# Kernel optimization log

Hardware: AMD Instinct MI355X
Metric: run time of the kernel (lower is better)

Reference implementation:

```python
import jax, jax.numpy as jnp
import numpy as np

D_MODEL = 768
NUM_HEADS = 12
D_K = D_MODEL // NUM_HEADS  # 64


def setup_inputs() -> dict:
    key = jax.random.key(0)
    ks = jax.random.split(key, 7)
    B, S = 2, 4096
    Q = jax.random.normal(ks[0], (B, S, D_MODEL), dtype=jnp.float32)
    K = jax.random.normal(ks[1], (B, S, D_MODEL), dtype=jnp.float32)
    V = jax.random.normal(ks[2], (B, S, D_MODEL), dtype=jnp.float32)
    scale = 1.0 / np.sqrt(D_MODEL)
    # Per-head projection weights stacked: [H, d_model, d_k] (equivalent to
    # the torch per-head nn.Linear(d_model, d_k, bias=False) applied as x @ W)
    WQ = jax.random.normal(ks[3], (NUM_HEADS, D_MODEL, D_K), dtype=jnp.float32) * scale
    WK = jax.random.normal(ks[4], (NUM_HEADS, D_MODEL, D_K), dtype=jnp.float32) * scale
    WV = jax.random.normal(ks[5], (NUM_HEADS, D_MODEL, D_K), dtype=jnp.float32) * scale
    # Output projection: [num_head*d_v, d_model]
    WO = jax.random.normal(ks[6], (NUM_HEADS * D_K, D_MODEL), dtype=jnp.float32) * scale
    return {"Q": Q, "K": K, "V": V, "WQ": WQ, "WK": WK, "WV": WV, "WO": WO}


def reference(Q, K, V, WQ, WK, WV, WO):
    # Per-head projections (batched over heads): [B,H,S,d_k]
    q = jnp.einsum('bsd,hdk->bhsk', Q, WQ)
    k = jnp.einsum('bsd,hdk->bhsk', K, WK)
    v = jnp.einsum('bsd,hdk->bhsk', V, WV)
    # Full attention scores: [B,H,S,S]
    scores = jnp.einsum('bhqd,bhsd->bhqs', q, k) / jnp.sqrt(jnp.asarray(D_K, q.dtype))
    attn = jax.nn.softmax(scores, axis=-1)  # dropout_p=0 -> identity
    out = jnp.einsum('bhqs,bhsd->bhqd', attn, v)  # [B,H,S,d_k]
    # Concatenate heads along feature dim (head order = concat order)
    B, H, S, Dk = out.shape
    out = out.transpose(0, 2, 1, 3).reshape(B, S, H * Dk)
    return out @ WO  # [B,S,d_model]
```

## Files before the change

kernel.cpp:

```cpp
#include <hip/hip_runtime.h>
#include <hip/hip_bf16.h>
#include <stdint.h>
#include <stddef.h>

#define NH 12
#define DKH 64
#define DM 768
#define SS 4096

typedef __attribute__((ext_vector_type(8))) short bf16x8;
typedef __attribute__((ext_vector_type(4))) float f32x4;
typedef __attribute__((ext_vector_type(16))) float f32x16;

__device__ __forceinline__ unsigned short f2bf(float x) {
  union { float f; unsigned int u; } a; a.f = x;
  unsigned int r = a.u + 0x7fffu + ((a.u >> 16) & 1u);
  return (unsigned short)(r >> 16);
}

__device__ __forceinline__ unsigned pkbf2(float a, float b) {
  union { __hip_bfloat162 h; unsigned u; } x;
  x.h = __float22bfloat162_rn(float2{a, b});
  return x.u;
}

__device__ __forceinline__ unsigned cvt_pk_bf16(float lo, float hi) {
  unsigned r;
  asm("v_cvt_pk_bf16_f32 %0, %1, %2" : "=v"(r) : "v"(lo), "v"(hi));
  return r;
}

__device__ __forceinline__ void plane32_swap(unsigned& a, unsigned& b) {
  asm("v_permlane32_swap_b32 %0, %1" : "+v"(a), "+v"(b));
}

__device__ __forceinline__ float fast_exp2(float x) {
#if __has_builtin(__builtin_amdgcn_exp2f)
  return __builtin_amdgcn_exp2f(x);
#else
  return exp2f(x);
#endif
}

__device__ __forceinline__ void gload16(const void* g, void* l) {
  __builtin_amdgcn_global_load_lds(
      (const __attribute__((address_space(1))) void*)g,
      (__attribute__((address_space(3))) void*)l, 16, 0, 0);
}

__global__ __launch_bounds__(256) void conv_weights(
    const float* __restrict__ WQ, const float* __restrict__ WK,
    const float* __restrict__ WV, const float* __restrict__ WO,
    unsigned short* __restrict__ wq, unsigned short* __restrict__ wk,
    unsigned short* __restrict__ wv, unsigned short* __restrict__ wo) {
  int idx = blockIdx.x * 256 + threadIdx.x;
  if (idx >= DM * DM) return;
  int n = idx / DM, k = idx % DM;
  int src = ((n >> 6) * DM + k) * DKH + (n & 63);
  wq[idx] = f2bf(WQ[src] * 0.18033688011112042f);
  wk[idx] = f2bf(WK[src]);
  wv[idx] = f2bf(WV[src]);
  wo[idx] = f2bf(WO[k * DM + n]);
}

__global__ __launch_bounds__(256) void qkv_conv(
    const float* __restrict__ Q, const float* __restrict__ K,
    const float* __restrict__ V, unsigned short* __restrict__ out) {
  int gid = blockIdx.x * 256 + threadIdx.x;
  int t = gid / 786432, e = gid % 786432;
  const float* src = (t == 0) ? Q : (t == 1) ? K : V;
  float4 a = *(const float4*)(src + (size_t)e * 8);
  float4 c = *(const float4*)(src + (size_t)e * 8 + 4);
  union { unsigned u[4]; uint4 v; } o;
  o.u[0] = pkbf2(a.x, a.y); o.u[1] = pkbf2(a.z, a.w);
  o.u[2] = pkbf2(c.x, c.y); o.u[3] = pkbf2(c.z, c.w);
  *(uint4*)(out + (size_t)t * 6291456 + (size_t)e * 8) = o.v;
}

__global__ __launch_bounds__(256, 2) void proj_gemm3(
    const unsigned short* __restrict__ Abase,
    const unsigned short* __restrict__ Wbase,
    unsigned short* __restrict__ Obase) {
  __shared__ unsigned short As[2][128 * 64];
  __shared__ unsigned short Bs[2][96 * 64];
  const int tid = threadIdx.x;
  const int lane = tid & 63, wave = tid >> 6;
  const int wm = wave >> 1, wn = wave & 1;
  const int l15 = lane & 15, lhi = lane >> 4;
  const int lrow = lane >> 3;
  const int schunk = (lane & 7) ^ lrow;

  int fid = blockIdx.x + (blockIdx.y << 3) + (blockIdx.z << 9);
  int nid = (fid & 7) * 192 + (fid >> 3);
  const int bx = nid & 7;
  const int rem = nid >> 3;
  const int by = rem & 63, z = rem >> 6;
  const bool z2 = (z == 2);

  const unsigned short* A = Abase + (size_t)z * 6291456;
  const unsigned short* Wt = Wbase + (size_t)z * DM * DM;
  unsigned short* out = Obase + (size_t)z * 2 * NH * SS * DKH;
  const int m0 = by * 128, n0 = bx * 96;

  auto stage = [&](int k0, int buf) {
#pragma unroll
    for (int i = 0; i < 4; ++i) {
      int r = wave * 32 + i * 8;
      gload16(A + (size_t)(m0 + r + lrow) * DM + k0 + schunk * 8, &As[buf][r * 64]);
    }
#pragma unroll
    for (int i = 0; i < 3; ++i) {
      int r = wave * 24 + i * 8;
      gload16(Wt + (size_t)(n0 + r + lrow) * DM + k0 + schunk * 8, &Bs[buf][r * 64]);
    }
  };

  f32x4 acc[4][3] = {};

  stage(0, 0);
  stage(64, 1);

  for (int t = 0; t < 12; ++t) {
    if (t < 11) asm volatile("s_waitcnt vmcnt(7)" ::: "memory");
    else        asm volatile("s_waitcnt vmcnt(0)" ::: "memory");
    asm volatile("s_barrier" ::: "memory");
    const int buf = t & 1;
    bf16x8 af[4][2], bfr[3][2];
#pragma unroll
    for (int m = 0; m < 4; ++m) {
      int row = wm * 64 + m * 16 + l15;
#pragma unroll
      for (int ks = 0; ks < 2; ++ks)
        af[m][ks] = *(const bf16x8*)&As[buf][row * 64 + (((ks * 4 + lhi) ^ (row & 7)) * 8)];
    }
#pragma unroll
    for (int n = 0; n < 3; ++n) {
      int row = wn * 48 + n * 16 + l15;
#pragma unroll
      for (int ks = 0; ks < 2; ++ks)
        bfr[n][ks] = *(const bf16x8*)&Bs[buf][row * 64 + (((ks * 4 + lhi) ^ (row & 7)) * 8)];
    }
    asm volatile("s_waitcnt lgkmcnt(0)" ::: "memory");
    asm volatile("s_barrier" ::: "memory");
    if (t + 2 < 12) stage((t + 2) * 64, buf);
    __builtin_amdgcn_s_setprio(1);
#pragma unroll
    for (int ks = 0; ks < 2; ++ks)
#pragma unroll
      for (int m = 0; m < 4; ++m)
#pragma unroll
        for (int n = 0; n < 3; ++n) {
          if (z2)
            acc[m][n] = __builtin_amdgcn_mfma_f32_16x16x32_bf16(bfr[n][ks], af[m][ks], acc[m][n], 0, 0, 0);
          else
            acc[m][n] = __builtin_amdgcn_mfma_f32_16x16x32_bf16(af[m][ks], bfr[n][ks], acc[m][n], 0, 0, 0);
        }
    __builtin_amdgcn_s_setprio(0);
  }

  if (!z2) {
#pragma unroll
    for (int m = 0; m < 4; ++m) {
#pragma unroll
      for (int r = 0; r < 4; ++r) {
        int row = m0 + wm * 64 + m * 16 + lhi * 4 + r;
        int bb = row >> 12, s = row & 4095;
#pragma unroll
        for (int n = 0; n < 3; ++n) {
          int col = n0 + wn * 48 + n * 16 + l15;
          int hh = col >> 6, dk = col & 63;
          out[((size_t)(bb * NH + hh) * SS + s) * DKH + dk] = f2bf(acc[m][n][r]);
        }
      }
    }
  } else {
#pragma unroll
    for (int m = 0; m < 4; ++m) {
      int srow = m0 + wm * 64 + m * 16 + l15;
      int bb = srow >> 12, s = srow & 4095;
#pragma unroll
      for (int n = 0; n < 3; ++n) {
#pragma unroll
        for (int r = 0; r < 4; ++r) {
          int col = n0 + wn * 48 + n * 16 + lhi * 4 + r;
          int hh = col >> 6, dk = col & 63;
          out[((size_t)(bb * NH + hh) * DKH + dk) * SS + s] = f2bf(acc[m][n][r]);
        }
      }
    }
  }
}

__device__ __forceinline__ void pack_pb(const f32x16& s0, const f32x16& s1, bf16x8* pb) {
#pragma unroll
  for (int h2 = 0; h2 < 2; ++h2) {
    unsigned c0a = cvt_pk_bf16(s0[8 * h2 + 0], s0[8 * h2 + 1]);
    unsigned c1a = cvt_pk_bf16(s0[8 * h2 + 2], s0[8 * h2 + 3]);
    unsigned c0b = cvt_pk_bf16(s0[8 * h2 + 4], s0[8 * h2 + 5]);
    unsigned c1b = cvt_pk_bf16(s0[8 * h2 + 6], s0[8 * h2 + 7]);
    plane32_swap(c0a, c0b);
    plane32_swap(c1a, c1b);
    union { unsigned u[4]; bf16x8 v; } f;
    f.u[0] = c0a; f.u[1] = c1a; f.u[2] = c0b; f.u[3] = c1b;
    pb[h2] = f.v;
  }
#pragma unroll
  for (int h2 = 0; h2 < 2; ++h2) {
    unsigned c0a = cvt_pk_bf16(s1[8 * h2 + 0], s1[8 * h2 + 1]);
    unsigned c1a = cvt_pk_bf16(s1[8 * h2 + 2], s1[8 * h2 + 3]);
    unsigned c0b = cvt_pk_bf16(s1[8 * h2 + 4], s1[8 * h2 + 5]);
    unsigned c1b = cvt_pk_bf16(s1[8 * h2 + 6], s1[8 * h2 + 7]);
    plane32_swap(c0a, c0b);
    plane32_swap(c1a, c1b);
    union { unsigned u[4]; bf16x8 v; } f;
    f.u[0] = c0a; f.u[1] = c1a; f.u[2] = c0b; f.u[3] = c1b;
    pb[2 + h2] = f.v;
  }
}

__device__ __forceinline__ float tree16(const f32x16& v) {
  float a = (v[0] + v[1]) + (v[2] + v[3]);
  float b = (v[4] + v[5]) + (v[6] + v[7]);
  float c = (v[8] + v[9]) + (v[10] + v[11]);
  float d = (v[12] + v[13]) + (v[14] + v[15]);
  return (a + b) + (c + d);
}

__global__ __launch_bounds__(128, 2) void flash_attn(
    const unsigned short* __restrict__ Qp, const unsigned short* __restrict__ Kp,
    const unsigned short* __restrict__ Vt, unsigned short* __restrict__ Ao) {
  __shared__ unsigned short KV[2][8192];
  const int tid = threadIdx.x;
  const int lane = tid & 63, wp = tid >> 6;
  const int ql = lane & 31, hi = lane >> 5;

  int fid = blockIdx.x + (blockIdx.y << 5);
  int nid = (fid & 7) * 96 + (fid >> 3);
  const int bx = nid & 31, bh = nid >> 5;
  const int b = bh / NH, h = bh % NH;
  const int q0 = bx * 128 + wp * 64;

  bf16x8 qf0[4], qf1[4];
  {
    const unsigned short* qb = Qp + ((size_t)bh * SS + q0 + ql) * DKH;
#pragma unroll
    for (int s = 0; s < 4; ++s) {
      qf0[s] = *(const bf16x8*)(qb + s * 16 + hi * 8);
      qf1[s] = *(const bf16x8*)(qb + 32 * DKH + s * 16 + hi * 8);
    }
  }

  const unsigned short* gK = Kp + (size_t)bh * SS * DKH;
  const unsigned short* gV = Vt + (size_t)bh * DKH * SS;
  const int lrow = lane >> 3;
  const int sch = ((lane & 7) ^ lrow) * 8;
  const int xs = (ql & 7) << 3;

  auto stage = [&](int kv0, int buf) {
#pragma unroll
    for (int i = 0; i < 4; ++i) {
      int r = wp * 32 + i * 8;
      gload16(gK + (size_t)(kv0 + r + lrow) * DKH + sch, &KV[buf][r * 64]);
      gload16(gV + (size_t)(r + lrow) * SS + kv0 + sch, &KV[buf][4096 + r * 64]);
    }
  };

  stage(0, 0);

  f32x16 oA = {}, oB = {}, oC = {}, oD = {};
  float lp0 = 0.f, lp1 = 0.f;

  for (int it = 0; it < 64; ++it) {
    asm volatile("s_waitcnt vmcnt(0)" ::: "memory");
    __builtin_amdgcn_s_barrier();
    __builtin_amdgcn_sched_barrier(0);
    const int buf = it & 1;
    if (it + 1 < 64) stage((it + 1) * 64, buf ^ 1);
    const unsigned short* Ks = &KV[buf][0];
    const unsigned short* Vs = &KV[buf][4096];

    f32x16 s00 = {}, s01 = {}, s10 = {}, s11 = {};
    __builtin_amdgcn_s_setprio(1);
#pragma unroll
    for (int s = 0; s < 4; ++s) {
      bf16x8 ka0 = *(const bf16x8*)&Ks[ql * 64 + ((s * 16 + hi * 8) ^ xs)];
      bf16x8 ka1 = *(const bf16x8*)&Ks[(32 + ql) * 64 + ((s * 16 + hi * 8) ^ xs)];
      s00 = __builtin_amdgcn_mfma_f32_32x32x16_bf16(ka0, qf0[s], s00, 0, 0, 0);
      s10 = __builtin_amdgcn_mfma_f32_32x32x16_bf16(ka0, qf1[s], s10, 0, 0, 0);
      s01 = __builtin_amdgcn_mfma_f32_32x32x16_bf16(ka1, qf0[s], s01, 0, 0, 0);
      s11 = __builtin_amdgcn_mfma_f32_32x32x16_bf16(ka1, qf1[s], s11, 0, 0, 0);
    }
    __builtin_amdgcn_s_setprio(0);

#pragma unroll
    for (int r = 0; r < 16; ++r) s00[r] = fast_exp2(s00[r]);
#pragma unroll
    for (int r = 0; r < 16; ++r) s01[r] = fast_exp2(s01[r]);
#pragma unroll
    for (int r = 0; r < 16; ++r) s10[r] = fast_exp2(s10[r]);
#pragma unroll
    for (int r = 0; r < 16; ++r) s11[r] = fast_exp2(s11[r]);
    lp0 += tree16(s00) + tree16(s01);
    lp1 += tree16(s10) + tree16(s11);

    bf16x8 pb0[4], pb1[4];
    pack_pb(s00, s01, pb0);
    pack_pb(s10, s11, pb1);

    __builtin_amdgcn_s_setprio(1);
#pragma unroll
    for (int ks = 0; ks < 4; ++ks) {
      bf16x8 va0 = *(const bf16x8*)&Vs[ql * 64 + ((ks * 16 + hi * 8) ^ xs)];
      bf16x8 va1 = *(const bf16x8*)&Vs[(32 + ql) * 64 + ((ks * 16 + hi * 8) ^ xs)];
      oA = __builtin_amdgcn_mfma_f32_32x32x16_bf16(va0, pb0[ks], oA, 0, 0, 0);
      oB = __builtin_amdgcn_mfma_f32_32x32x16_bf16(va1, pb0[ks], oB, 0, 0, 0);
      oC = __builtin_amdgcn_mfma_f32_32x32x16_bf16(va0, pb1[ks], oC, 0, 0, 0);
      oD = __builtin_amdgcn_mfma_f32_32x32x16_bf16(va1, pb1[ks], oD, 0, 0, 0);
    }
    __builtin_amdgcn_s_setprio(0);
  }

  float inv0 = 1.0f / (lp0 + __shfl_xor(lp0, 32));
  float inv1 = 1.0f / (lp1 + __shfl_xor(lp1, 32));
  unsigned short* orow0 = Ao + ((size_t)b * SS + q0 + ql) * DM + h * DKH;
  unsigned short* orow1 = Ao + ((size_t)b * SS + q0 + 32 + ql) * DM + h * DKH;
#pragma unroll
  for (int g = 0; g < 4; ++g) {
    int d0 = g * 8 + hi * 4;
    *(unsigned*)&orow0[d0]          = cvt_pk_bf16(oA[4 * g + 0] * inv0, oA[4 * g + 1] * inv0);
    *(unsigned*)&orow0[d0 + 2]      = cvt_pk_bf16(oA[4 * g + 2] * inv0, oA[4 * g + 3] * inv0);
    *(unsigned*)&orow0[32 + d0]     = cvt_pk_bf16(oB[4 * g + 0] * inv0, oB[4 * g + 1] * inv0);
    *(unsigned*)&orow0[32 + d0 + 2] = cvt_pk_bf16(oB[4 * g + 2] * inv0, oB[4 * g + 3] * inv0);
    *(unsigned*)&orow1[d0]          = cvt_pk_bf16(oC[4 * g + 0] * inv1, oC[4 * g + 1] * inv1);
    *(unsigned*)&orow1[d0 + 2]      = cvt_pk_bf16(oC[4 * g + 2] * inv1, oC[4 * g + 3] * inv1);
    *(unsigned*)&orow1[32 + d0]     = cvt_pk_bf16(oD[4 * g + 0] * inv1, oD[4 * g + 1] * inv1);
    *(unsigned*)&orow1[32 + d0 + 2] = cvt_pk_bf16(oD[4 * g + 2] * inv1, oD[4 * g + 3] * inv1);
  }
}

__global__ __launch_bounds__(256, 2) void out_gemm(
    const unsigned short* __restrict__ A, const unsigned short* __restrict__ Wt,
    float* __restrict__ out) {
  __shared__ unsigned short As[2][64 * 64];
  __shared__ unsigned short Bs[2][128 * 64];
  const int tid = threadIdx.x;
  const int lane = tid & 63, wave = tid >> 6;
  const int wm = wave >> 1, wn = wave & 1;
  const int l15 = lane & 15, lhi = lane >> 4;
  const int lrow = lane >> 3;
  const int schunk = (lane & 7) ^ lrow;

  int fid = blockIdx.x + 6 * blockIdx.y;
  int nid = (fid & 7) * 96 + (fid >> 3);
  const int bx = nid % 6, by = nid / 6;
  const int m0 = by * 64, n0 = bx * 128;

  auto stage = [&](int k0, int buf) {
#pragma unroll
    for (int i = 0; i < 4; ++i) {
      int r = wave * 32 + i * 8;
      gload16(Wt + (size_t)(n0 + r + lrow) * DM + k0 + schunk * 8, &Bs[buf][r * 64]);
    }
#pragma unroll
    for (int i = 0; i < 2; ++i) {
      int r = wave * 16 + i * 8;
      gload16(A + (size_t)(m0 + r + lrow) * DM + k0 + schunk * 8, &As[buf][r * 64]);
    }
  };

  f32x4 acc[2][4] = {};
  stage(0, 0);
  stage(64, 1);

  for (int t = 0; t < 12; ++t) {
    if (t < 11) asm volatile("s_waitcnt vmcnt(6)" ::: "memory");
    else        asm volatile("s_waitcnt vmcnt(0)" ::: "memory");
    asm volatile("s_barrier" ::: "memory");
    const int buf = t & 1;
    bf16x8 af[2][2], bfr[4][2];
#pragma unroll
    for (int m = 0; m < 2; ++m) {
      int row = wm * 32 + m * 16 + l15;
#pragma unroll
      for (int ks = 0; ks < 2; ++ks)
        af[m][ks] = *(const bf16x8*)&As[buf][row * 64 + (((ks * 4 + lhi) ^ (row & 7)) * 8)];
    }
#pragma unroll
    for (int n = 0; n < 4; ++n) {
      int row = wn * 64 + n * 16 + l15;
#pragma unroll
      for (int ks = 0; ks < 2; ++ks)
        bfr[n][ks] = *(const bf16x8*)&Bs[buf][row * 64 + (((ks * 4 + lhi) ^ (row & 7)) * 8)];
    }
    asm volatile("s_waitcnt lgkmcnt(0)" ::: "memory");
    asm volatile("s_barrier" ::: "memory");
    if (t + 2 < 12) stage((t + 2) * 64, buf);
    __builtin_amdgcn_s_setprio(1);
#pragma unroll
    for (int ks = 0; ks < 2; ++ks)
#pragma unroll
      for (int m = 0; m < 2; ++m)
#pragma unroll
        for (int n = 0; n < 4; ++n)
          acc[m][n] = __builtin_amdgcn_mfma_f32_16x16x32_bf16(af[m][ks], bfr[n][ks], acc[m][n], 0, 0, 0);
    __builtin_amdgcn_s_setprio(0);
  }

#pragma unroll
  for (int m = 0; m < 2; ++m)
#pragma unroll
    for (int r = 0; r < 4; ++r) {
      int row = m0 + wm * 32 + m * 16 + lhi * 4 + r;
#pragma unroll
      for (int n = 0; n < 4; ++n) {
        int col = n0 + wn * 64 + n * 16 + l15;
        out[(size_t)row * DM + col] = acc[m][n][r];
      }
    }
}

extern "C" void kernel_launch(void* const* d_in, const int* in_sizes, int n_in,
                              void* d_out, int out_size, void* d_ws, size_t ws_size,
                              hipStream_t stream) {
  const float* Q  = (const float*)d_in[0];
  const float* K  = (const float*)d_in[1];
  const float* V  = (const float*)d_in[2];
  const float* WQ = (const float*)d_in[3];
  const float* WK = (const float*)d_in[4];
  const float* WV = (const float*)d_in[5];
  const float* WO = (const float*)d_in[6];
  char* ws = (char*)d_ws;

  const size_t WSZ = (size_t)DM * DM * 2;
  const size_t ABF = (size_t)2 * SS * DM * 2;
  unsigned short* w_base  = (unsigned short*)(ws);
  unsigned short* wo_t    = (unsigned short*)(ws + 3 * WSZ);
  unsigned short* qkv_bf  = (unsigned short*)(ws + 4 * WSZ);
  unsigned short* p_base  = (unsigned short*)(ws + 4 * WSZ + 3 * ABF);
  unsigned short* q_p  = p_base;
  unsigned short* k_p  = p_base + ABF / 2;
  unsigned short* v_t  = p_base + ABF;
  unsigned short* attn = p_base + 3 * (ABF / 2);

  conv_weights<<<(DM * DM + 255) / 256, 256, 0, stream>>>(
      WQ, WK, WV, WO, w_base, w_base + WSZ / 2, w_base + WSZ, wo_t);

  qkv_conv<<<9216, 256, 0, stream>>>(Q, K, V, qkv_bf);

  proj_gemm3<<<dim3(8, 64, 3), 256, 0, stream>>>(qkv_bf, w_base, p_base);

  flash_attn<<<dim3(32, 24), 128, 0, stream>>>(q_p, k_p, v_t, attn);

  out_gemm<<<dim3(6, 128), 256, 0, stream>>>(attn, wo_t, (float*)d_out);
}
```

Baseline: 221.5 us.

## Restructure flash attention to register-resident K, single-buffered V, 4 waves

Flash attention now uses 4 waves of 32 query rows each instead of 2 waves of 64. Each wave loads K fragments straight from global memory into registers, prefetching the next tile. Only V is staged in a single LDS buffer, refreshed after a barrier. This shrinks LDS use and register footprint so more blocks can be resident, at the cost of redundant K reads from global/L2 across waves and extra barriers per iteration. The two conversion kernels are also merged into a single launch to save one launch.

```diff
diff --git a/kernel.cpp b/kernel.cpp
--- a/kernel.cpp
+++ b/kernel.cpp
@@ -48,33 +48,34 @@
       (__attribute__((address_space(3))) void*)l, 16, 0, 0);
 }
 
-__global__ __launch_bounds__(256) void conv_weights(
-    const float* __restrict__ WQ, const float* __restrict__ WK,
-    const float* __restrict__ WV, const float* __restrict__ WO,
+__global__ __launch_bounds__(256) void prep(
+    const float* __restrict__ Q, const float* __restrict__ K,
+    const float* __restrict__ V, const float* __restrict__ WQ,
+    const float* __restrict__ WK, const float* __restrict__ WV,
+    const float* __restrict__ WO, unsigned short* __restrict__ qkv,
     unsigned short* __restrict__ wq, unsigned short* __restrict__ wk,
     unsigned short* __restrict__ wv, unsigned short* __restrict__ wo) {
-  int idx = blockIdx.x * 256 + threadIdx.x;
-  if (idx >= DM * DM) return;
-  int n = idx / DM, k = idx % DM;
-  int src = ((n >> 6) * DM + k) * DKH + (n & 63);
-  wq[idx] = f2bf(WQ[src] * 0.18033688011112042f);
-  wk[idx] = f2bf(WK[src]);
-  wv[idx] = f2bf(WV[src]);
-  wo[idx] = f2bf(WO[k * DM + n]);
-}
-
-__global__ __launch_bounds__(256) void qkv_conv(
-    const float* __restrict__ Q, const float* __restrict__ K,
-    const float* __restrict__ V, unsigned short* __restrict__ out) {
-  int gid = blockIdx.x * 256 + threadIdx.x;
-  int t = gid / 786432, e = gid % 786432;
-  const float* src = (t == 0) ? Q : (t == 1) ? K : V;
-  float4 a = *(const float4*)(src + (size_t)e * 8);
-  float4 c = *(const float4*)(src + (size_t)e * 8 + 4);
-  union { unsigned u[4]; uint4 v; } o;
-  o.u[0] = pkbf2(a.x, a.y); o.u[1] = pkbf2(a.z, a.w);
-  o.u[2] = pkbf2(c.x, c.y); o.u[3] = pkbf2(c.z, c.w);
-  *(uint4*)(out + (size_t)t * 6291456 + (size_t)e * 8) = o.v;
+  int bx = blockIdx.x;
+  if (bx < 9216) {
+    int gid = bx * 256 + threadIdx.x;
+    int t = gid / 786432, e = gid % 786432;
+    const float* src = (t == 0) ? Q : (t == 1) ? K : V;
+    float4 a = *(const float4*)(src + (size_t)e * 8);
+    float4 c = *(const float4*)(src + (size_t)e * 8 + 4);
+    union { unsigned u[4]; uint4 v; } o;
+    o.u[0] = pkbf2(a.x, a.y); o.u[1] = pkbf2(a.z, a.w);
+    o.u[2] = pkbf2(c.x, c.y); o.u[3] = pkbf2(c.z, c.w);
+    *(uint4*)(qkv + (size_t)t * 6291456 + (size_t)e * 8) = o.v;
+  } else {
+    int idx = (bx - 9216) * 256 + threadIdx.x;
+    if (idx >= DM * DM) return;
+    int n = idx / DM, k = idx % DM;
+    int src = ((n >> 6) * DM + k) * DKH + (n & 63);
+    wq[idx] = f2bf(WQ[src] * 0.18033688011112042f);
+    wk[idx] = f2bf(WK[src]);
+    wv[idx] = f2bf(WV[src]);
+    wo[idx] = f2bf(WO[k * DM + n]);
+  }
 }
 
 __global__ __launch_bounds__(256, 2) void proj_gemm3(
@@ -226,28 +227,26 @@
   return (a + b) + (c + d);
 }
 
-__global__ __launch_bounds__(128, 2) void flash_attn(
+__global__ __launch_bounds__(256, 3) void flash_attn(
     const unsigned short* __restrict__ Qp, const unsigned short* __restrict__ Kp,
     const unsigned short* __restrict__ Vt, unsigned short* __restrict__ Ao) {
-  __shared__ unsigned short KV[2][8192];
+  __shared__ unsigned short Vs[4096];
   const int tid = threadIdx.x;
-  const int lane = tid & 63, wp = tid >> 6;
+  const int lane = tid & 63, wave = tid >> 6;
   const int ql = lane & 31, hi = lane >> 5;
 
   int fid = blockIdx.x + (blockIdx.y << 5);
   int nid = (fid & 7) * 96 + (fid >> 3);
   const int bx = nid & 31, bh = nid >> 5;
   const int b = bh / NH, h = bh % NH;
-  const int q0 = bx * 128 + wp * 64;
-
-  bf16x8 qf0[4], qf1[4];
+  const int q0w = bx * 128 + wave * 32;
+
+  bf16x8 qf[4];
   {
-    const unsigned short* qb = Qp + ((size_t)bh * SS + q0 + ql) * DKH;
-#pragma unroll
-    for (int s = 0; s < 4; ++s) {
-      qf0[s] = *(const bf16x8*)(qb + s * 16 + hi * 8);
-      qf1[s] = *(const bf16x8*)(qb + 32 * DKH + s * 16 + hi * 8);
-    }
+    const unsigned short* qb = Qp + ((size_t)bh * SS + q0w + ql) * DKH;
+#pragma unroll
+    for (int s = 0; s < 4; ++s)
+      qf[s] = *(const bf16x8*)(qb + s * 16 + hi * 8);
   }
 
   const unsigned short* gK = Kp + (size_t)bh * SS * DKH;
@@ -255,86 +254,88 @@
   const int lrow = lane >> 3;
   const int sch = ((lane & 7) ^ lrow) * 8;
   const int xs = (ql & 7) << 3;
-
-  auto stage = [&](int kv0, int buf) {
-#pragma unroll
-    for (int i = 0; i < 4; ++i) {
-      int r = wp * 32 + i * 8;
-      gload16(gK + (size_t)(kv0 + r + lrow) * DKH + sch, &KV[buf][r * 64]);
-      gload16(gV + (size_t)(r + lrow) * SS + kv0 + sch, &KV[buf][4096 + r * 64]);
+  const unsigned short* pkb = gK + (size_t)ql * DKH + hi * 8;
+
+  bf16x8 kf0[4], kf1[4];
+  auto loadK = [&](int kv0) {
+    const unsigned short* pk = pkb + (size_t)kv0 * DKH;
+#pragma unroll
+    for (int s = 0; s < 4; ++s) {
+      kf0[s] = *(const bf16x8*)(pk + s * 16);
+      kf1[s] = *(const bf16x8*)(pk + 2048 + s * 16);
     }
   };
-
-  stage(0, 0);
-
-  f32x16 oA = {}, oB = {}, oC = {}, oD = {};
-  float lp0 = 0.f, lp1 = 0.f;
+  auto stageV = [&](int kv0) {
+#pragma unroll
+    for (int i = 0; i < 2; ++i) {
+      int r = wave * 16 + i * 8;
+      gload16(gV + (size_t)(r + lrow) * SS + kv0 + sch, &Vs[r * 64]);
+    }
+  };
+
+  loadK(0);
+  stageV(0);
+
+  f32x16 oA = {}, oB = {};
+  float lp = 0.f;
+  const f32x16 zc = {};
 
   for (int it = 0; it < 64; ++it) {
-    asm volatile("s_waitcnt vmcnt(0)" ::: "memory");
-    __builtin_amdgcn_s_barrier();
+    const bool notlast = (it < 63);
+    f32x16 s0, s1;
+    __builtin_amdgcn_s_setprio(1);
+    s0 = __builtin_amdgcn_mfma_f32_32x32x16_bf16(kf0[0], qf[0], zc, 0, 0, 0);
+    s1 = __builtin_amdgcn_mfma_f32_32x32x16_bf16(kf1[0], qf[0], zc, 0, 0, 0);
+#pragma unroll
+    for (int s = 1; s < 4; ++s) {
+      s0 = __builtin_amdgcn_mfma_f32_32x32x16_bf16(kf0[s], qf[s], s0, 0, 0, 0);
+      s1 = __builtin_amdgcn_mfma_f32_32x32x16_bf16(kf1[s], qf[s], s1, 0, 0, 0);
+    }
+    __builtin_amdgcn_s_setprio(0);
     __builtin_amdgcn_sched_barrier(0);
-    const int buf = it & 1;
-    if (it + 1 < 64) stage((it + 1) * 64, buf ^ 1);
-    const unsigned short* Ks = &KV[buf][0];
-    const unsigned short* Vs = &KV[buf][4096];
-
-    f32x16 s00 = {}, s01 = {}, s10 = {}, s11 = {};
-    __builtin_amdgcn_s_setprio(1);
-#pragma unroll
-    for (int s = 0; s < 4; ++s) {
-      bf16x8 ka0 = *(const bf16x8*)&Ks[ql * 64 + ((s * 16 + hi * 8) ^ xs)];
-      bf16x8 ka1 = *(const bf16x8*)&Ks[(32 + ql) * 64 + ((s * 16 + hi * 8) ^ xs)];
-      s00 = __builtin_amdgcn_mfma_f32_32x32x16_bf16(ka0, qf0[s], s00, 0, 0, 0);
-      s10 = __builtin_amdgcn_mfma_f32_32x32x16_bf16(ka0, qf1[s], s10, 0, 0, 0);
-      s01 = __builtin_amdgcn_mfma_f32_32x32x16_bf16(ka1, qf0[s], s01, 0, 0, 0);
-      s11 = __builtin_amdgcn_mfma_f32_32x32x16_bf16(ka1, qf1[s], s11, 0, 0, 0);
-    }
-    __builtin_amdgcn_s_setprio(0);
-
-#pragma unroll
-    for (int r = 0; r < 16; ++r) s00[r] = fast_exp2(s00[r]);
-#pragma unroll
-    for (int r = 0; r < 16; ++r) s01[r] = fast_exp2(s01[r]);
-#pragma unroll
-    for (int r = 0; r < 16; ++r) s10[r] = fast_exp2(s10[r]);
-#pragma unroll
-    for (int r = 0; r < 16; ++r) s11[r] = fast_exp2(s11[r]);
-    lp0 += tree16(s00) + tree16(s01);
-    lp1 += tree16(s10) + tree16(s11);
-
-    bf16x8 pb0[4], pb1[4];
-    pack_pb(s00, s01, pb0);
-    pack_pb(s10, s11, pb1);
+    if (notlast) loadK((it + 1) * 64);
+    __builtin_amdgcn_sched_barrier(0);
+
+#pragma unroll
+    for (int r = 0; r < 16; ++r) s0[r] = fast_exp2(s0[r]);
+#pragma unroll
+    for (int r = 0; r < 16; ++r) s1[r] = fast_exp2(s1[r]);
+    lp += tree16(s0) + tree16(s1);
+
+    bf16x8 pb[4];
+    pack_pb(s0, s1, pb);
+
+    if (notlast) asm volatile("s_waitcnt vmcnt(8)" ::: "memory");
+    else         asm volatile("s_waitcnt vmcnt(0)" ::: "memory");
+    asm volatile("s_barrier" ::: "memory");
+    __builtin_amdgcn_sched_barrier(0);
 
     __builtin_amdgcn_s_setprio(1);
 #pragma unroll
     for (int ks = 0; ks < 4; ++ks) {
       bf16x8 va0 = *(const bf16x8*)&Vs[ql * 64 + ((ks * 16 + hi * 8) ^ xs)];
       bf16x8 va1 = *(const bf16x8*)&Vs[(32 + ql) * 64 + ((ks * 16 + hi * 8) ^ xs)];
-      oA = __builtin_amdgcn_mfma_f32_32x32x16_bf16(va0, pb0[ks], oA, 0, 0, 0);
-      oB = __builtin_amdgcn_mfma_f32_32x32x16_bf16(va1, pb0[ks], oB, 0, 0, 0);
-      oC = __builtin_amdgcn_mfma_f32_32x32x16_bf16(va0, pb1[ks], oC, 0, 0, 0);
-      oD = __builtin_amdgcn_mfma_f32_32x32x16_bf16(va1, pb1[ks], oD, 0, 0, 0);
+      oA = __builtin_amdgcn_mfma_f32_32x32x16_bf16(va0, pb[ks], oA, 0, 0, 0);
+      oB = __builtin_amdgcn_mfma_f32_32x32x16_bf16(va1, pb[ks], oB, 0, 0, 0);
     }
     __builtin_amdgcn_s_setprio(0);
-  }
-
-  float inv0 = 1.0f / (lp0 + __shfl_xor(lp0, 32));
-  float inv1 = 1.0f / (lp1 + __shfl_xor(lp1, 32));
-  unsigned short* orow0 = Ao + ((size_t)b * SS + q0 + ql) * DM + h * DKH;
-  unsigned short* orow1 = Ao + ((size_t)b * SS + q0 + 32 + ql) * DM + h * DKH;
+
+    if (notlast) {
+      asm volatile("s_waitcnt lgkmcnt(0)" ::: "memory");
+      asm volatile("s_barrier" ::: "memory");
+      stageV((it + 1) * 64);
+    }
+  }
+
+  float inv = 1.0f / (lp + __shfl_xor(lp, 32));
+  unsigned short* orow = Ao + ((size_t)b * SS + q0w + ql) * DM + h * DKH;
 #pragma unroll
   for (int g = 0; g < 4; ++g) {
     int d0 = g * 8 + hi * 4;
-    *(unsigned*)&orow0[d0]          = cvt_pk_bf16(oA[4 * g + 0] * inv0, oA[4 * g + 1] * inv0);
-    *(unsigned*)&orow0[d0 + 2]      = cvt_pk_bf16(oA[4 * g + 2] * inv0, oA[4 * g + 3] * inv0);
-    *(unsigned*)&orow0[32 + d0]     = cvt_pk_bf16(oB[4 * g + 0] * inv0, oB[4 * g + 1] * inv0);
-    *(unsigned*)&orow0[32 + d0 + 2] = cvt_pk_bf16(oB[4 * g + 2] * inv0, oB[4 * g + 3] * inv0);
-    *(unsigned*)&orow1[d0]          = cvt_pk_bf16(oC[4 * g + 0] * inv1, oC[4 * g + 1] * inv1);
-    *(unsigned*)&orow1[d0 + 2]      = cvt_pk_bf16(oC[4 * g + 2] * inv1, oC[4 * g + 3] * inv1);
-    *(unsigned*)&orow1[32 + d0]     = cvt_pk_bf16(oD[4 * g + 0] * inv1, oD[4 * g + 1] * inv1);
-    *(unsigned*)&orow1[32 + d0 + 2] = cvt_pk_bf16(oD[4 * g + 2] * inv1, oD[4 * g + 3] * inv1);
+    *(unsigned*)&orow[d0]          = cvt_pk_bf16(oA[4 * g + 0] * inv, oA[4 * g + 1] * inv);
+    *(unsigned*)&orow[d0 + 2]      = cvt_pk_bf16(oA[4 * g + 2] * inv, oA[4 * g + 3] * inv);
+    *(unsigned*)&orow[32 + d0]     = cvt_pk_bf16(oB[4 * g + 0] * inv, oB[4 * g + 1] * inv);
+    *(unsigned*)&orow[32 + d0 + 2] = cvt_pk_bf16(oB[4 * g + 2] * inv, oB[4 * g + 3] * inv);
   }
 }
 
@@ -442,14 +443,13 @@
   unsigned short* v_t  = p_base + ABF;
   unsigned short* attn = p_base + 3 * (ABF / 2);
 
-  conv_weights<<<(DM * DM + 255) / 256, 256, 0, stream>>>(
-      WQ, WK, WV, WO, w_base, w_base + WSZ / 2, w_base + WSZ, wo_t);
-
-  qkv_conv<<<9216, 256, 0, stream>>>(Q, K, V, qkv_bf);
+  prep<<<9216 + 2304, 256, 0, stream>>>(
+      Q, K, V, WQ, WK, WV, WO, qkv_bf,
+      w_base, w_base + WSZ / 2, w_base + WSZ, wo_t);
 
   proj_gemm3<<<dim3(8, 64, 3), 256, 0, stream>>>(qkv_bf, w_base, p_base);
 
-  flash_attn<<<dim3(32, 24), 128, 0, stream>>>(q_p, k_p, v_t, attn);
+  flash_attn<<<dim3(32, 24), 256, 0, stream>>>(q_p, k_p, v_t, attn);
 
   out_gemm<<<dim3(6, 128), 256, 0, stream>>>(attn, wo_t, (float*)d_out);
 }
```

Result: slower. 284.2 us (+28.3%).
